# Optimization experiments

Hardware: AMD Instinct MI355X
Metric: run time of the kernel (lower is better)

The kernel has to match this reference:

```python
import jax, jax.numpy as jnp
import numpy as np

EPS = 1e-7  # keras.backend.epsilon()
ROUTINGS = 3


def _squash(s):
    # s: [B, k, d]; squash over last (capsule-dim) axis, matching squash(..., axis=-2)
    # applied to [B,1,k,d,1] in the original.
    ss = jnp.sum(s * s, axis=-1, keepdims=True) + EPS
    return (jnp.sqrt(ss) / (1.0 + ss)) * s


def setup_inputs() -> dict:
    key = jax.random.key(0)
    kx, kw, km = jax.random.split(key, 3)
    B, n, k, d = 32, 2048, 32, 16
    x = jax.random.normal(kx, (B, n, d), dtype=jnp.float32)
    # glorot-ish scale for W: fan ~ d
    W = jax.random.normal(kw, (1, n, k, d, d), dtype=jnp.float32) * (1.0 / np.sqrt(d))
    mu0 = jax.random.uniform(km, (B, k, d), dtype=jnp.float32)  # np.random.rand equivalent
    return {"x": x, "W": W, "mu0": mu0}


def reference(x, W, mu0):
    B, n, d = x.shape
    k = mu0.shape[1]
    pi = jnp.full((B, k), 1.0 / k, dtype=x.dtype)
    mu = mu0
    sigma = jnp.ones((B, k, d), dtype=x.dtype)
    log2pi = jnp.log(2.0 * jnp.pi).astype(x.dtype)
    R = jnp.zeros((B, n, k), dtype=x.dtype)
    for _ in range(ROUTINGS):
        # E-step: gamma[b,k,n] = pi_k * N(x_n | mu_k, diag(sigma_k^2)), normalized over k.
        z = (x[:, None, :, :] - mu[:, :, None, :]) / sigma[:, :, None, :]  # [B,k,n,d]
        logN = -0.5 * (jnp.sum(z * z, axis=-1) + d * log2pi) - jnp.sum(jnp.log(sigma), axis=-1)[:, :, None]
        gamma = jax.nn.softmax(jnp.log(pi)[:, :, None] + logN, axis=1)  # [B,k,n]
        R = jnp.transpose(gamma, (0, 2, 1))  # [B,n,k]
        # M-step
        N_k = jnp.sum(R, axis=1)  # [B,k]
        pi = N_k / n
        mu = jnp.einsum('bnk,bnd->bkd', R, x) / N_k[:, :, None]
        diff2 = (x[:, None, :, :] - mu[:, :, None, :]) ** 2  # [B,k,n,d]
        sigma = jnp.sqrt(jnp.einsum('bkn,bknd->bkd', gamma, diff2) / N_k[:, :, None])
    # caps_predicted[b,n,k,d] = W[0,n,k,d,:] @ x[b,n,:]
    caps_pred = jnp.einsum('nkde,bne->bnkd', W[0], x)
    s = jnp.sum(caps_pred * R[..., None], axis=1)  # [B,k,d]
    return _squash(s)
```

## Files before the change

kernel.cpp:

```cpp
#include <hip/hip_runtime.h>
#include <hip/hip_bf16.h>
#include <math.h>

#define BN 32
#define NN 2048
#define KK 32
#define DD 16
#define SC 32
#define ACC_C 4
#define ACC_STRIDE 33792


typedef __attribute__((ext_vector_type(8))) short bf16x8;
typedef __attribute__((ext_vector_type(16))) float f32x16;

static __device__ __forceinline__ ushort f2bf(float f) {
    unsigned int u = __float_as_uint(f);
    return (ushort)((u + 0x7FFFu + ((u >> 16) & 1u)) >> 16);
}

__global__ void k_zero(float4* __restrict__ p) {
    int i = blockIdx.x * 256 + threadIdx.x;
    p[i] = make_float4(0.f, 0.f, 0.f, 0.f);
}

template <int MODE, int FIRST>
__global__ __launch_bounds__(256, 4) void k_estep(
    const float* __restrict__ x, const float* __restrict__ mu0,
    const float* __restrict__ accIn, float* __restrict__ accOut,
    float* __restrict__ Rout) {
    const int b = blockIdx.x >> 5;
    const int chunk = blockIdx.x & 31;
    const int tid = threadIdx.x;
    const int wave = tid >> 6;
    const int lane = tid & 63;
    const int k = lane & 31;
    const int jj = lane >> 5;

    float mk[DD], ik[DD], ck;
    if (FIRST) {
        const float4* mp = (const float4*)(mu0 + (size_t)(b * KK + k) * DD);
#pragma unroll
        for (int q = 0; q < 4; q++) {
            float4 m4 = mp[q];
            mk[q*4+0]=m4.x; mk[q*4+1]=m4.y; mk[q*4+2]=m4.z; mk[q*4+3]=m4.w;
        }
#pragma unroll
        for (int d = 0; d < DD; d++) ik[d] = 1.0f;
        ck = -3.4657359028f;
    } else {
        float N = 0.f, sxv[DD], sxxv[DD];
#pragma unroll
        for (int d = 0; d < DD; d++) { sxv[d] = 0.f; sxxv[d] = 0.f; }
#pragma unroll
        for (int c = 0; c < ACC_C; c++) {
            const float* base = accIn + (size_t)c * ACC_STRIDE;
            N += base[b * KK + k];
            const float4* sxp  = (const float4*)(base + 1024  + (size_t)(b * KK + k) * DD);
            const float4* sxxp = (const float4*)(base + 17408 + (size_t)(b * KK + k) * DD);
#pragma unroll
            for (int q = 0; q < 4; q++) {
                float4 a = sxp[q], c2 = sxxp[q];
                sxv[q*4+0]+=a.x; sxv[q*4+1]+=a.y; sxv[q*4+2]+=a.z; sxv[q*4+3]+=a.w;
                sxxv[q*4+0]+=c2.x; sxxv[q*4+1]+=c2.y; sxxv[q*4+2]+=c2.z; sxxv[q*4+3]+=c2.w;
            }
        }
        float invN = 1.0f / N;
        float sumlog = 0.f;
#pragma unroll
        for (int d = 0; d < DD; d++) {
            float m_ = sxv[d] * invN;
            float v = fmaxf(sxxv[d] * invN - m_ * m_, 1e-12f);
            mk[d] = m_;
            ik[d] = rsqrtf(v);
            sumlog += __logf(v);
        }
        ck = __logf(N * (1.0f / NN)) - 0.5f * sumlog;
    }

    float aN = 0.f, aSx[DD], aSxx[DD];
#pragma unroll
    for (int d = 0; d < DD; d++) { aSx[d] = 0.f; aSxx[d] = 0.f; }

#pragma unroll 4
    for (int i = 0; i < 8; i++) {
        const int n = chunk * 64 + i * 8 + wave * 2 + jj;
        const float4* xp = (const float4*)(x + ((size_t)b * NN + n) * DD);
        float xv[DD];
#pragma unroll
        for (int q = 0; q < 4; q++) {
            float4 v = xp[q];
            xv[q*4+0]=v.x; xv[q*4+1]=v.y; xv[q*4+2]=v.z; xv[q*4+3]=v.w;
        }
        float qd = 0.f;
#pragma unroll
        for (int d = 0; d < DD; d++) {
            float z = (xv[d] - mk[d]) * ik[d];
            qd = fmaf(z, z, qd);
        }
        float logit = ck - 0.5f * qd;
        float m = logit;
#pragma unroll
        for (int off = 1; off < 32; off <<= 1) m = fmaxf(m, __shfl_xor(m, off));
        float e = __expf(logit - m);
        float ssum = e;
#pragma unroll
        for (int off = 1; off < 32; off <<= 1) ssum += __shfl_xor(ssum, off);
        float g = e / ssum;

        if (MODE == 1) {
            Rout[((size_t)b * NN + n) * KK + k] = g;
        } else {
            aN += g;
#pragma unroll
            for (int d = 0; d < DD; d++) {
                aSx[d] = fmaf(g, xv[d], aSx[d]);
                aSxx[d] = fmaf(g * xv[d], xv[d], aSxx[d]);
            }
        }
    }

    if (MODE == 0) {
        __shared__ float red[4][KK * 33];
        aN += __shfl_xor(aN, 32);
#pragma unroll
        for (int d = 0; d < DD; d++) {
            aSx[d] += __shfl_xor(aSx[d], 32);
            aSxx[d] += __shfl_xor(aSxx[d], 32);
        }
        if (jj == 0) {
            red[wave][k * 33 + 0] = aN;
#pragma unroll
            for (int d = 0; d < DD; d++) {
                red[wave][k * 33 + 1 + d] = aSx[d];
                red[wave][k * 33 + 17 + d] = aSxx[d];
            }
        }
        __syncthreads();
        float* outc = accOut + (size_t)(chunk & (ACC_C - 1)) * ACC_STRIDE;
        for (int idx = tid; idx < KK * 33; idx += 256) {
            float v = red[0][idx] + red[1][idx] + red[2][idx] + red[3][idx];
            int kk2 = idx / 33, j = idx % 33;
            float* dst;
            if (j == 0) dst = outc + b * KK + kk2;
            else if (j < 17) dst = outc + 1024 + (size_t)(b * KK + kk2) * DD + (j - 1);
            else dst = outc + 17408 + (size_t)(b * KK + kk2) * DD + (j - 17);
            unsafeAtomicAdd(dst, v);
        }
    }
}

__global__ __launch_bounds__(256) void k_xpack(const float* __restrict__ x,
                                               ushort* __restrict__ xpk) {
    int idx = blockIdx.x * 256 + threadIdx.x;
    int n = idx >> 6, l = idx & 63;
    int b = l & 31, e0 = (l >> 5) * 8;
    const float4* xp = (const float4*)(x + ((size_t)b * NN + n) * DD + e0);
    float4 a = xp[0], c = xp[1];
    ushort* o = xpk + (size_t)idx * 8;
    o[0]=f2bf(a.x); o[1]=f2bf(a.y); o[2]=f2bf(a.z); o[3]=f2bf(a.w);
    o[4]=f2bf(c.x); o[5]=f2bf(c.y); o[6]=f2bf(c.z); o[7]=f2bf(c.w);
}

__global__ __launch_bounds__(256, 4) void k_caps(
    const float* __restrict__ W, const ushort* __restrict__ xpk,
    const float* __restrict__ R, float* __restrict__ s) {
    const int tid = threadIdx.x;
    const int wv = tid >> 6, l = tid & 63;
    const int chunk = blockIdx.x >> 2, tg = blockIdx.x & 3;
    const int t = tg * 4 + wv;
    const int col = l & 31, hi = l >> 5;
    const int kq = (l >> 4) & 1;
    float* sc = s + (size_t)(chunk & (SC - 1)) * (BN * KK * DD);

    float sacc[16];
#pragma unroll
    for (int q = 0; q < 16; q++) sacc[q] = 0.f;
    const f32x16 zacc = {0.f,0.f,0.f,0.f, 0.f,0.f,0.f,0.f,
                         0.f,0.f,0.f,0.f, 0.f,0.f,0.f,0.f};

#pragma unroll 2
    for (int i = 0; i < 8; i++) {
        const int n = chunk * 8 + i;
        bf16x8 af = *(const bf16x8*)(xpk + ((size_t)n * 64 + l) * 8);
        const float4* wp = (const float4*)(W + (((size_t)n * 512 + t * 32 + col) * DD) + hi * 8);
        float4 wlo = wp[0], whi = wp[1];
        bf16x8 bfr;
        bfr[0]=(short)f2bf(wlo.x); bfr[1]=(short)f2bf(wlo.y);
        bfr[2]=(short)f2bf(wlo.z); bfr[3]=(short)f2bf(wlo.w);
        bfr[4]=(short)f2bf(whi.x); bfr[5]=(short)f2bf(whi.y);
        bfr[6]=(short)f2bf(whi.z); bfr[7]=(short)f2bf(whi.w);
        const float* rn = R + (size_t)(4 * hi) * (NN * KK) + (size_t)n * KK + 2 * t + kq;
        float r0  = rn[(size_t) 0 * (NN * KK)];
        float r1  = rn[(size_t) 1 * (NN * KK)];
        float r2  = rn[(size_t) 2 * (NN * KK)];
        float r3  = rn[(size_t) 3 * (NN * KK)];
        float r4  = rn[(size_t) 8 * (NN * KK)];
        float r5  = rn[(size_t) 9 * (NN * KK)];
        float r6  = rn[(size_t)10 * (NN * KK)];
        float r7  = rn[(size_t)11 * (NN * KK)];
        float r8  = rn[(size_t)16 * (NN * KK)];
        float r9  = rn[(size_t)17 * (NN * KK)];
        float r10 = rn[(size_t)18 * (NN * KK)];
        float r11 = rn[(size_t)19 * (NN * KK)];
        float r12 = rn[(size_t)24 * (NN * KK)];
        float r13 = rn[(size_t)25 * (NN * KK)];
        float r14 = rn[(size_t)26 * (NN * KK)];
        float r15 = rn[(size_t)27 * (NN * KK)];

        f32x16 D = __builtin_amdgcn_mfma_f32_32x32x16_bf16(af, bfr, zacc, 0, 0, 0);

        sacc[0]  = fmaf(r0,  D[0],  sacc[0]);
        sacc[1]  = fmaf(r1,  D[1],  sacc[1]);
        sacc[2]  = fmaf(r2,  D[2],  sacc[2]);
        sacc[3]  = fmaf(r3,  D[3],  sacc[3]);
        sacc[4]  = fmaf(r4,  D[4],  sacc[4]);
        sacc[5]  = fmaf(r5,  D[5],  sacc[5]);
        sacc[6]  = fmaf(r6,  D[6],  sacc[6]);
        sacc[7]  = fmaf(r7,  D[7],  sacc[7]);
        sacc[8]  = fmaf(r8,  D[8],  sacc[8]);
        sacc[9]  = fmaf(r9,  D[9],  sacc[9]);
        sacc[10] = fmaf(r10, D[10], sacc[10]);
        sacc[11] = fmaf(r11, D[11], sacc[11]);
        sacc[12] = fmaf(r12, D[12], sacc[12]);
        sacc[13] = fmaf(r13, D[13], sacc[13]);
        sacc[14] = fmaf(r14, D[14], sacc[14]);
        sacc[15] = fmaf(r15, D[15], sacc[15]);
    }

    const int kd = t * 32 + col;
#pragma unroll
    for (int q = 0; q < 16; q++) {
        const int b = (q & 3) + 8 * (q >> 2) + 4 * hi;
        unsafeAtomicAdd(sc + (size_t)b * (KK * DD) + kd, sacc[q]);
    }
}

__global__ void k_squash(const float* __restrict__ s, float* __restrict__ out) {
    int idx = blockIdx.x * 256 + threadIdx.x;
    float v = 0.f;
#pragma unroll 8
    for (int c = 0; c < SC; c++) v += s[(size_t)c * (BN * KK * DD) + idx];
    float ss = v * v;
#pragma unroll
    for (int off = 1; off < 16; off <<= 1) ss += __shfl_xor(ss, off);
    ss += 1e-7f;
    float scale = sqrtf(ss) / (1.0f + ss);
    out[idx] = v * scale;
}

extern "C" void kernel_launch(void* const* d_in, const int* in_sizes, int n_in,
                              void* d_out, int out_size, void* d_ws, size_t ws_size,
                              hipStream_t stream) {
    const float* x   = (const float*)d_in[0];
    const float* W   = (const float*)d_in[1];
    const float* mu0 = (const float*)d_in[2];
    float* ws   = (float*)d_ws;
    float* accA = ws;
    float* accB = ws + 135168;
    float* s    = ws + 270336;
    float* R    = ws + 794624;
    ushort* xpk = (ushort*)(ws + 2891776);

    k_zero<<<776, 256, 0, stream>>>((float4*)ws);

    k_xpack<<<512, 256, 0, stream>>>(x, xpk);

    k_estep<0, 1><<<1024, 256, 0, stream>>>(x, mu0, nullptr, accA, nullptr);
    k_estep<0, 0><<<1024, 256, 0, stream>>>(x, nullptr, accA, accB, nullptr);
    k_estep<1, 0><<<1024, 256, 0, stream>>>(x, nullptr, accB, nullptr, R);

    k_caps<<<1024, 256, 0, stream>>>(W, xpk, R, s);
    k_squash<<<64, 256, 0, stream>>>(s, (float*)d_out);
}
```

Measured before the change: 96.79 us.

## Split EM E-step into per-point gamma, moment and parameter kernels

Result: slower. 126.2 us (+30.4%).

```diff
diff --git a/kernel.cpp b/kernel.cpp
--- a/kernel.cpp
+++ b/kernel.cpp
@@ -9,6 +9,7 @@
 #define SC 32
 #define ACC_C 4
 #define ACC_STRIDE 33792
+#define PRM_STRIDE 36
 
 
 typedef __attribute__((ext_vector_type(8))) short bf16x8;
@@ -18,73 +19,102 @@
     unsigned int u = __float_as_uint(f);
     return (ushort)((u + 0x7FFFu + ((u >> 16) & 1u)) >> 16);
 }
+static __device__ __forceinline__ short f2bfs(float f) {
+    __hip_bfloat16 h = __float2bfloat16(f);
+    return *reinterpret_cast<short*>(&h);
+}
 
 __global__ void k_zero(float4* __restrict__ p) {
     int i = blockIdx.x * 256 + threadIdx.x;
     p[i] = make_float4(0.f, 0.f, 0.f, 0.f);
 }
 
-template <int MODE, int FIRST>
-__global__ __launch_bounds__(256, 4) void k_estep(
+template <int FIRST>
+__global__ __launch_bounds__(256) void k_gamma(
     const float* __restrict__ x, const float* __restrict__ mu0,
-    const float* __restrict__ accIn, float* __restrict__ accOut,
-    float* __restrict__ Rout) {
-    const int b = blockIdx.x >> 5;
-    const int chunk = blockIdx.x & 31;
+    const float* __restrict__ prm, float* __restrict__ R) {
+    const int b = blockIdx.x >> 3;
+    const int n = (blockIdx.x & 7) * 256 + threadIdx.x;
+
+    float xv[DD];
+    {
+        const float4* xp = (const float4*)(x + ((size_t)b * NN + n) * DD);
+#pragma unroll
+        for (int q = 0; q < 4; q++) {
+            float4 v = xp[q];
+            xv[q*4+0]=v.x; xv[q*4+1]=v.y; xv[q*4+2]=v.z; xv[q*4+3]=v.w;
+        }
+    }
+
+    float l[KK];
+    float m = -3.0e38f;
+#pragma unroll
+    for (int k = 0; k < KK; k++) {
+        float qd = 0.f, ck;
+        if (FIRST) {
+            const float4* mp = (const float4*)(mu0 + (size_t)(b * KK + k) * DD);
+#pragma unroll
+            for (int q = 0; q < 4; q++) {
+                float4 m4 = mp[q];
+                float z0 = xv[q*4+0] - m4.x, z1 = xv[q*4+1] - m4.y;
+                float z2 = xv[q*4+2] - m4.z, z3 = xv[q*4+3] - m4.w;
+                qd = fmaf(z0, z0, qd); qd = fmaf(z1, z1, qd);
+                qd = fmaf(z2, z2, qd); qd = fmaf(z3, z3, qd);
+            }
+            ck = -3.4657359028f;
+        } else {
+            const float* pp = prm + (size_t)(b * KK + k) * PRM_STRIDE;
+            const float4* mp = (const float4*)pp;
+            const float4* ip = (const float4*)(pp + 16);
+#pragma unroll
+            for (int q = 0; q < 4; q++) {
+                float4 m4 = mp[q], i4 = ip[q];
+                float z0 = (xv[q*4+0] - m4.x) * i4.x;
+                float z1 = (xv[q*4+1] - m4.y) * i4.y;
+                float z2 = (xv[q*4+2] - m4.z) * i4.z;
+                float z3 = (xv[q*4+3] - m4.w) * i4.w;
+                qd = fmaf(z0, z0, qd); qd = fmaf(z1, z1, qd);
+                qd = fmaf(z2, z2, qd); qd = fmaf(z3, z3, qd);
+            }
+            ck = pp[32];
+        }
+        l[k] = ck - 0.5f * qd;
+        m = fmaxf(m, l[k]);
+    }
+    float ssum = 0.f;
+#pragma unroll
+    for (int k = 0; k < KK; k++) {
+        float e = __expf(l[k] - m);
+        ssum += e;
+        l[k] = e;
+    }
+    const float inv = 1.0f / ssum;
+    float4* Rr = (float4*)(R + ((size_t)b * NN + n) * KK);
+#pragma unroll
+    for (int q = 0; q < 8; q++) {
+        float4 v = make_float4(l[q*4+0]*inv, l[q*4+1]*inv, l[q*4+2]*inv, l[q*4+3]*inv);
+        Rr[q] = v;
+    }
+}
+
+__global__ __launch_bounds__(256, 4) void k_moments(
+    const float* __restrict__ x, const float* __restrict__ R,
+    float* __restrict__ accOut) {
+    const int b = blockIdx.x >> 4;
+    const int chunk = blockIdx.x & 15;
     const int tid = threadIdx.x;
     const int wave = tid >> 6;
     const int lane = tid & 63;
     const int k = lane & 31;
     const int jj = lane >> 5;
 
-    float mk[DD], ik[DD], ck;
-    if (FIRST) {
-        const float4* mp = (const float4*)(mu0 + (size_t)(b * KK + k) * DD);
-#pragma unroll
-        for (int q = 0; q < 4; q++) {
-            float4 m4 = mp[q];
-            mk[q*4+0]=m4.x; mk[q*4+1]=m4.y; mk[q*4+2]=m4.z; mk[q*4+3]=m4.w;
-        }
-#pragma unroll
-        for (int d = 0; d < DD; d++) ik[d] = 1.0f;
-        ck = -3.4657359028f;
-    } else {
-        float N = 0.f, sxv[DD], sxxv[DD];
-#pragma unroll
-        for (int d = 0; d < DD; d++) { sxv[d] = 0.f; sxxv[d] = 0.f; }
-#pragma unroll
-        for (int c = 0; c < ACC_C; c++) {
-            const float* base = accIn + (size_t)c * ACC_STRIDE;
-            N += base[b * KK + k];
-            const float4* sxp  = (const float4*)(base + 1024  + (size_t)(b * KK + k) * DD);
-            const float4* sxxp = (const float4*)(base + 17408 + (size_t)(b * KK + k) * DD);
-#pragma unroll
-            for (int q = 0; q < 4; q++) {
-                float4 a = sxp[q], c2 = sxxp[q];
-                sxv[q*4+0]+=a.x; sxv[q*4+1]+=a.y; sxv[q*4+2]+=a.z; sxv[q*4+3]+=a.w;
-                sxxv[q*4+0]+=c2.x; sxxv[q*4+1]+=c2.y; sxxv[q*4+2]+=c2.z; sxxv[q*4+3]+=c2.w;
-            }
-        }
-        float invN = 1.0f / N;
-        float sumlog = 0.f;
-#pragma unroll
-        for (int d = 0; d < DD; d++) {
-            float m_ = sxv[d] * invN;
-            float v = fmaxf(sxxv[d] * invN - m_ * m_, 1e-12f);
-            mk[d] = m_;
-            ik[d] = rsqrtf(v);
-            sumlog += __logf(v);
-        }
-        ck = __logf(N * (1.0f / NN)) - 0.5f * sumlog;
-    }
-
     float aN = 0.f, aSx[DD], aSxx[DD];
 #pragma unroll
     for (int d = 0; d < DD; d++) { aSx[d] = 0.f; aSxx[d] = 0.f; }
 
 #pragma unroll 4
-    for (int i = 0; i < 8; i++) {
-        const int n = chunk * 64 + i * 8 + wave * 2 + jj;
+    for (int i = 0; i < 16; i++) {
+        const int n = chunk * 128 + i * 8 + wave * 2 + jj;
         const float4* xp = (const float4*)(x + ((size_t)b * NN + n) * DD);
         float xv[DD];
 #pragma unroll
@@ -92,62 +122,74 @@
             float4 v = xp[q];
             xv[q*4+0]=v.x; xv[q*4+1]=v.y; xv[q*4+2]=v.z; xv[q*4+3]=v.w;
         }
-        float qd = 0.f;
+        float g = R[((size_t)b * NN + n) * KK + k];
+        aN += g;
 #pragma unroll
         for (int d = 0; d < DD; d++) {
-            float z = (xv[d] - mk[d]) * ik[d];
-            qd = fmaf(z, z, qd);
-        }
-        float logit = ck - 0.5f * qd;
-        float m = logit;
-#pragma unroll
-        for (int off = 1; off < 32; off <<= 1) m = fmaxf(m, __shfl_xor(m, off));
-        float e = __expf(logit - m);
-        float ssum = e;
-#pragma unroll
-        for (int off = 1; off < 32; off <<= 1) ssum += __shfl_xor(ssum, off);
-        float g = e / ssum;
-
-        if (MODE == 1) {
-            Rout[((size_t)b * NN + n) * KK + k] = g;
-        } else {
-            aN += g;
-#pragma unroll
-            for (int d = 0; d < DD; d++) {
-                aSx[d] = fmaf(g, xv[d], aSx[d]);
-                aSxx[d] = fmaf(g * xv[d], xv[d], aSxx[d]);
-            }
-        }
-    }
-
-    if (MODE == 0) {
-        __shared__ float red[4][KK * 33];
-        aN += __shfl_xor(aN, 32);
+            aSx[d] = fmaf(g, xv[d], aSx[d]);
+            aSxx[d] = fmaf(g * xv[d], xv[d], aSxx[d]);
+        }
+    }
+
+    __shared__ float red[4][KK * 33];
+    aN += __shfl_xor(aN, 32);
+#pragma unroll
+    for (int d = 0; d < DD; d++) {
+        aSx[d] += __shfl_xor(aSx[d], 32);
+        aSxx[d] += __shfl_xor(aSxx[d], 32);
+    }
+    if (jj == 0) {
+        red[wave][k * 33 + 0] = aN;
 #pragma unroll
         for (int d = 0; d < DD; d++) {
-            aSx[d] += __shfl_xor(aSx[d], 32);
-            aSxx[d] += __shfl_xor(aSxx[d], 32);
-        }
-        if (jj == 0) {
-            red[wave][k * 33 + 0] = aN;
-#pragma unroll
-            for (int d = 0; d < DD; d++) {
-                red[wave][k * 33 + 1 + d] = aSx[d];
-                red[wave][k * 33 + 17 + d] = aSxx[d];
-            }
-        }
-        __syncthreads();
-        float* outc = accOut + (size_t)(chunk & (ACC_C - 1)) * ACC_STRIDE;
-        for (int idx = tid; idx < KK * 33; idx += 256) {
-            float v = red[0][idx] + red[1][idx] + red[2][idx] + red[3][idx];
-            int kk2 = idx / 33, j = idx % 33;
-            float* dst;
-            if (j == 0) dst = outc + b * KK + kk2;
-            else if (j < 17) dst = outc + 1024 + (size_t)(b * KK + kk2) * DD + (j - 1);
-            else dst = outc + 17408 + (size_t)(b * KK + kk2) * DD + (j - 17);
-            unsafeAtomicAdd(dst, v);
-        }
-    }
+            red[wave][k * 33 + 1 + d] = aSx[d];
+            red[wave][k * 33 + 17 + d] = aSxx[d];
+        }
+    }
+    __syncthreads();
+    float* outc = accOut + (size_t)(chunk & (ACC_C - 1)) * ACC_STRIDE;
+    for (int idx = tid; idx < KK * 33; idx += 256) {
+        float v = red[0][idx] + red[1][idx] + red[2][idx] + red[3][idx];
+        int kk2 = idx / 33, j = idx % 33;
+        float* dst;
+        if (j == 0) dst = outc + b * KK + kk2;
+        else if (j < 17) dst = outc + 1024 + (size_t)(b * KK + kk2) * DD + (j - 1);
+        else dst = outc + 17408 + (size_t)(b * KK + kk2) * DD + (j - 17);
+        unsafeAtomicAdd(dst, v);
+    }
+}
+
+__global__ void k_param(const float* __restrict__ accIn, float* __restrict__ prm) {
+    int i = blockIdx.x * 256 + threadIdx.x;
+    if (i >= BN * KK) return;
+    float N = 0.f, sxv[DD], sxxv[DD];
+#pragma unroll
+    for (int d = 0; d < DD; d++) { sxv[d] = 0.f; sxxv[d] = 0.f; }
+#pragma unroll
+    for (int c = 0; c < ACC_C; c++) {
+        const float* base = accIn + (size_t)c * ACC_STRIDE;
+        N += base[i];
+        const float4* sxp  = (const float4*)(base + 1024  + (size_t)i * DD);
+        const float4* sxxp = (const float4*)(base + 17408 + (size_t)i * DD);
+#pragma unroll
+        for (int q = 0; q < 4; q++) {
+            float4 a = sxp[q], c2 = sxxp[q];
+            sxv[q*4+0]+=a.x; sxv[q*4+1]+=a.y; sxv[q*4+2]+=a.z; sxv[q*4+3]+=a.w;
+            sxxv[q*4+0]+=c2.x; sxxv[q*4+1]+=c2.y; sxxv[q*4+2]+=c2.z; sxxv[q*4+3]+=c2.w;
+        }
+    }
+    float invN = 1.0f / N;
+    float sumlog = 0.f;
+    float* pp = prm + (size_t)i * PRM_STRIDE;
+#pragma unroll
+    for (int d = 0; d < DD; d++) {
+        float m_ = sxv[d] * invN;
+        float v = fmaxf(sxxv[d] * invN - m_ * m_, 1e-12f);
+        pp[d] = m_;
+        pp[16 + d] = rsqrtf(v);
+        sumlog += __logf(v);
+    }
+    pp[32] = __logf(N * (1.0f / NN)) - 0.5f * sumlog;
 }
 
 __global__ __launch_bounds__(256) void k_xpack(const float* __restrict__ x,
@@ -179,17 +221,17 @@
     const f32x16 zacc = {0.f,0.f,0.f,0.f, 0.f,0.f,0.f,0.f,
                          0.f,0.f,0.f,0.f, 0.f,0.f,0.f,0.f};
 
-#pragma unroll 2
+#pragma unroll 4
     for (int i = 0; i < 8; i++) {
         const int n = chunk * 8 + i;
         bf16x8 af = *(const bf16x8*)(xpk + ((size_t)n * 64 + l) * 8);
         const float4* wp = (const float4*)(W + (((size_t)n * 512 + t * 32 + col) * DD) + hi * 8);
         float4 wlo = wp[0], whi = wp[1];
         bf16x8 bfr;
-        bfr[0]=(short)f2bf(wlo.x); bfr[1]=(short)f2bf(wlo.y);
-        bfr[2]=(short)f2bf(wlo.z); bfr[3]=(short)f2bf(wlo.w);
-        bfr[4]=(short)f2bf(whi.x); bfr[5]=(short)f2bf(whi.y);
-        bfr[6]=(short)f2bf(whi.z); bfr[7]=(short)f2bf(whi.w);
+        bfr[0]=f2bfs(wlo.x); bfr[1]=f2bfs(wlo.y);
+        bfr[2]=f2bfs(wlo.z); bfr[3]=f2bfs(wlo.w);
+        bfr[4]=f2bfs(whi.x); bfr[5]=f2bfs(whi.y);
+        bfr[6]=f2bfs(whi.z); bfr[7]=f2bfs(whi.w);
         const float* rn = R + (size_t)(4 * hi) * (NN * KK) + (size_t)n * KK + 2 * t + kq;
         float r0  = rn[(size_t) 0 * (NN * KK)];
         float r1  = rn[(size_t) 1 * (NN * KK)];
@@ -259,16 +301,20 @@
     float* accA = ws;
     float* accB = ws + 135168;
     float* s    = ws + 270336;
-    float* R    = ws + 794624;
-    ushort* xpk = (ushort*)(ws + 2891776);
+    float* prm  = ws + 794624;
+    float* R    = ws + 831488;
+    ushort* xpk = (ushort*)(ws + 2928640);
 
     k_zero<<<776, 256, 0, stream>>>((float4*)ws);
-
     k_xpack<<<512, 256, 0, stream>>>(x, xpk);
 
-    k_estep<0, 1><<<1024, 256, 0, stream>>>(x, mu0, nullptr, accA, nullptr);
-    k_estep<0, 0><<<1024, 256, 0, stream>>>(x, nullptr, accA, accB, nullptr);
-    k_estep<1, 0><<<1024, 256, 0, stream>>>(x, nullptr, accB, nullptr, R);
+    k_gamma<1><<<256, 256, 0, stream>>>(x, mu0, nullptr, R);
+    k_moments<<<512, 256, 0, stream>>>(x, R, accA);
+    k_param<<<4, 256, 0, stream>>>(accA, prm);
+    k_gamma<0><<<256, 256, 0, stream>>>(x, nullptr, prm, R);
+    k_moments<<<512, 256, 0, stream>>>(x, R, accB);
+    k_param<<<4, 256, 0, stream>>>(accB, prm);
+    k_gamma<0><<<256, 256, 0, stream>>>(x, nullptr, prm, R);
 
     k_caps<<<1024, 256, 0, stream>>>(W, xpk, R, s);
     k_squash<<<64, 256, 0, stream>>>(s, (float*)d_out);
```

## Replace atomic accumulation with per-block partial buffers and fuse launches

Applied to the files above, without the earlier changes.

After: 100.4 us. +3.8%, slower.

```diff
diff --git a/kernel.cpp b/kernel.cpp
--- a/kernel.cpp
+++ b/kernel.cpp
@@ -6,9 +6,9 @@
 #define NN 2048
 #define KK 32
 #define DD 16
-#define SC 32
-#define ACC_C 4
-#define ACC_STRIDE 33792
+#define PART_C 16
+#define PART_STRIDE 1056
+#define SCAPS 256
 
 
 typedef __attribute__((ext_vector_type(8))) short bf16x8;
@@ -19,18 +19,13 @@
     return (ushort)((u + 0x7FFFu + ((u >> 16) & 1u)) >> 16);
 }
 
-__global__ void k_zero(float4* __restrict__ p) {
-    int i = blockIdx.x * 256 + threadIdx.x;
-    p[i] = make_float4(0.f, 0.f, 0.f, 0.f);
-}
-
 template <int MODE, int FIRST>
-__global__ __launch_bounds__(256, 4) void k_estep(
-    const float* __restrict__ x, const float* __restrict__ mu0,
-    const float* __restrict__ accIn, float* __restrict__ accOut,
+static __device__ __forceinline__ void estep_body(
+    int blk, const float* __restrict__ x, const float* __restrict__ mu0,
+    const float* __restrict__ partIn, float* __restrict__ partOut,
     float* __restrict__ Rout) {
-    const int b = blockIdx.x >> 5;
-    const int chunk = blockIdx.x & 31;
+    const int b = blk >> 4;
+    const int chunk = blk & 15;
     const int tid = threadIdx.x;
     const int wave = tid >> 6;
     const int lane = tid & 63;
@@ -53,16 +48,13 @@
 #pragma unroll
         for (int d = 0; d < DD; d++) { sxv[d] = 0.f; sxxv[d] = 0.f; }
 #pragma unroll
-        for (int c = 0; c < ACC_C; c++) {
-            const float* base = accIn + (size_t)c * ACC_STRIDE;
-            N += base[b * KK + k];
-            const float4* sxp  = (const float4*)(base + 1024  + (size_t)(b * KK + k) * DD);
-            const float4* sxxp = (const float4*)(base + 17408 + (size_t)(b * KK + k) * DD);
-#pragma unroll
-            for (int q = 0; q < 4; q++) {
-                float4 a = sxp[q], c2 = sxxp[q];
-                sxv[q*4+0]+=a.x; sxv[q*4+1]+=a.y; sxv[q*4+2]+=a.z; sxv[q*4+3]+=a.w;
-                sxxv[q*4+0]+=c2.x; sxxv[q*4+1]+=c2.y; sxxv[q*4+2]+=c2.z; sxxv[q*4+3]+=c2.w;
+        for (int c = 0; c < PART_C; c++) {
+            const float* base = partIn + (size_t)(b * PART_C + c) * PART_STRIDE;
+            N += base[k];
+#pragma unroll
+            for (int d = 0; d < DD; d++) {
+                sxv[d]  += base[(1 + d) * 32 + k];
+                sxxv[d] += base[(17 + d) * 32 + k];
             }
         }
         float invN = 1.0f / N;
@@ -83,8 +75,8 @@
     for (int d = 0; d < DD; d++) { aSx[d] = 0.f; aSxx[d] = 0.f; }
 
 #pragma unroll 4
-    for (int i = 0; i < 8; i++) {
-        const int n = chunk * 64 + i * 8 + wave * 2 + jj;
+    for (int i = 0; i < 16; i++) {
+        const int n = chunk * 128 + i * 8 + wave * 2 + jj;
         const float4* xp = (const float4*)(x + ((size_t)b * NN + n) * DD);
         float xv[DD];
 #pragma unroll
@@ -137,22 +129,19 @@
             }
         }
         __syncthreads();
-        float* outc = accOut + (size_t)(chunk & (ACC_C - 1)) * ACC_STRIDE;
+        float* outp = partOut + (size_t)(b * PART_C + chunk) * PART_STRIDE;
         for (int idx = tid; idx < KK * 33; idx += 256) {
-            float v = red[0][idx] + red[1][idx] + red[2][idx] + red[3][idx];
-            int kk2 = idx / 33, j = idx % 33;
-            float* dst;
-            if (j == 0) dst = outc + b * KK + kk2;
-            else if (j < 17) dst = outc + 1024 + (size_t)(b * KK + kk2) * DD + (j - 1);
-            else dst = outc + 17408 + (size_t)(b * KK + kk2) * DD + (j - 17);
-            unsafeAtomicAdd(dst, v);
-        }
-    }
-}
-
-__global__ __launch_bounds__(256) void k_xpack(const float* __restrict__ x,
-                                               ushort* __restrict__ xpk) {
-    int idx = blockIdx.x * 256 + threadIdx.x;
+            int kk = idx & 31, j = idx >> 5;
+            float v = red[0][kk * 33 + j] + red[1][kk * 33 + j] +
+                      red[2][kk * 33 + j] + red[3][kk * 33 + j];
+            outp[idx] = v;
+        }
+    }
+}
+
+static __device__ __forceinline__ void xpack_body(int blk, const float* __restrict__ x,
+                                                  ushort* __restrict__ xpk) {
+    int idx = blk * 256 + threadIdx.x;
     int n = idx >> 6, l = idx & 63;
     int b = l & 31, e0 = (l >> 5) * 8;
     const float4* xp = (const float4*)(x + ((size_t)b * NN + n) * DD + e0);
@@ -160,6 +149,22 @@
     ushort* o = xpk + (size_t)idx * 8;
     o[0]=f2bf(a.x); o[1]=f2bf(a.y); o[2]=f2bf(a.z); o[3]=f2bf(a.w);
     o[4]=f2bf(c.x); o[5]=f2bf(c.y); o[6]=f2bf(c.z); o[7]=f2bf(c.w);
+}
+
+__global__ __launch_bounds__(256, 4) void k_fused1(
+    const float* __restrict__ x, const float* __restrict__ mu0,
+    float* __restrict__ partOut, ushort* __restrict__ xpk) {
+    if (blockIdx.x < 512)
+        estep_body<0, 1>(blockIdx.x, x, mu0, nullptr, partOut, nullptr);
+    else
+        xpack_body(blockIdx.x - 512, x, xpk);
+}
+
+template <int MODE>
+__global__ __launch_bounds__(256, 4) void k_estep(
+    const float* __restrict__ x, const float* __restrict__ partIn,
+    float* __restrict__ partOut, float* __restrict__ Rout) {
+    estep_body<MODE, 0>(blockIdx.x, x, nullptr, partIn, partOut, Rout);
 }
 
 __global__ __launch_bounds__(256, 4) void k_caps(
@@ -171,7 +176,7 @@
     const int t = tg * 4 + wv;
     const int col = l & 31, hi = l >> 5;
     const int kq = (l >> 4) & 1;
-    float* sc = s + (size_t)(chunk & (SC - 1)) * (BN * KK * DD);
+    float* sc = s + (size_t)chunk * (BN * KK * DD);
 
     float sacc[16];
 #pragma unroll
@@ -179,7 +184,7 @@
     const f32x16 zacc = {0.f,0.f,0.f,0.f, 0.f,0.f,0.f,0.f,
                          0.f,0.f,0.f,0.f, 0.f,0.f,0.f,0.f};
 
-#pragma unroll 2
+#pragma unroll 4
     for (int i = 0; i < 8; i++) {
         const int n = chunk * 8 + i;
         bf16x8 af = *(const bf16x8*)(xpk + ((size_t)n * 64 + l) * 8);
@@ -232,7 +237,7 @@
 #pragma unroll
     for (int q = 0; q < 16; q++) {
         const int b = (q & 3) + 8 * (q >> 2) + 4 * hi;
-        unsafeAtomicAdd(sc + (size_t)b * (KK * DD) + kd, sacc[q]);
+        sc[(size_t)b * (KK * DD) + kd] = sacc[q];
     }
 }
 
@@ -240,7 +245,7 @@
     int idx = blockIdx.x * 256 + threadIdx.x;
     float v = 0.f;
 #pragma unroll 8
-    for (int c = 0; c < SC; c++) v += s[(size_t)c * (BN * KK * DD) + idx];
+    for (int c = 0; c < SCAPS; c++) v += s[(size_t)c * (BN * KK * DD) + idx];
     float ss = v * v;
 #pragma unroll
     for (int off = 1; off < 16; off <<= 1) ss += __shfl_xor(ss, off);
@@ -255,21 +260,16 @@
     const float* x   = (const float*)d_in[0];
     const float* W   = (const float*)d_in[1];
     const float* mu0 = (const float*)d_in[2];
-    float* ws   = (float*)d_ws;
-    float* accA = ws;
-    float* accB = ws + 135168;
-    float* s    = ws + 270336;
-    float* R    = ws + 794624;
-    ushort* xpk = (ushort*)(ws + 2891776);
-
-    k_zero<<<776, 256, 0, stream>>>((float4*)ws);
-
-    k_xpack<<<512, 256, 0, stream>>>(x, xpk);
-
-    k_estep<0, 1><<<1024, 256, 0, stream>>>(x, mu0, nullptr, accA, nullptr);
-    k_estep<0, 0><<<1024, 256, 0, stream>>>(x, nullptr, accA, accB, nullptr);
-    k_estep<1, 0><<<1024, 256, 0, stream>>>(x, nullptr, accB, nullptr, R);
-
+    float* ws    = (float*)d_ws;
+    float* partA = ws;
+    float* partB = ws + 540672;
+    float* s     = ws + 1081344;
+    float* R     = ws + 5275648;
+    ushort* xpk  = (ushort*)(ws + 7372800);
+
+    k_fused1<<<1024, 256, 0, stream>>>(x, mu0, partA, xpk);
+    k_estep<0><<<512, 256, 0, stream>>>(x, partA, partB, nullptr);
+    k_estep<1><<<512, 256, 0, stream>>>(x, partB, nullptr, R);
     k_caps<<<1024, 256, 0, stream>>>(W, xpk, R, s);
     k_squash<<<64, 256, 0, stream>>>(s, (float*)d_out);
 }
```
